# Optimization experiments

Hardware: AMD Instinct MI355X
Metric: run time of the kernel (lower is better)

Reference implementation:

```python
import jax, jax.numpy as jnp
import numpy as np

B, MT, D, H, DEPTH, FF = 1024, 64, 512, 8, 4, 2048
HD = D // H
N_OBJ, N_TRI = 8192, 10240
NUM_OBJ_VOCAB, NUM_PRED_VOCAB = 180, 47


def setup_inputs() -> dict:
    key = jax.random.key(0)
    ks = jax.random.split(key, 20)
    s = 0.02
    inp = {}
    inp["objs"] = jax.random.randint(ks[0], (N_OBJ,), 0, NUM_OBJ_VOCAB)
    inp["boxes"] = jax.random.uniform(ks[1], (N_OBJ, 4), dtype=jnp.float32)
    inp["triples"] = jax.random.randint(ks[2], (N_TRI, 3), 0, NUM_PRED_VOCAB)
    inp["obj_to_img"] = jnp.sort(jax.random.randint(ks[3], (N_OBJ,), 0, B))
    inp["triple_to_img"] = jnp.sort(jax.random.randint(ks[4], (N_TRI,), 0, B))
    inp["obj_emb"] = jax.random.normal(ks[5], (NUM_OBJ_VOCAB, D), jnp.float32) * s
    inp["pred_emb"] = jax.random.normal(ks[6], (NUM_PRED_VOCAB, D), jnp.float32) * s
    inp["bw1"] = jax.random.normal(ks[7], (4, D), jnp.float32) * s
    inp["bb1"] = jnp.zeros((D,), jnp.float32)
    inp["blg"] = jnp.ones((D,), jnp.float32)
    inp["blb"] = jnp.zeros((D,), jnp.float32)
    inp["bw2"] = jax.random.normal(ks[8], (D, D), jnp.float32) * s
    inp["bb2"] = jnp.zeros((D,), jnp.float32)
    inp["ln1g"] = jnp.ones((DEPTH, D), jnp.float32)
    inp["ln1b"] = jnp.zeros((DEPTH, D), jnp.float32)
    inp["wq"] = jax.random.normal(ks[9], (DEPTH, D, D), jnp.float32) * s
    inp["bq"] = jnp.zeros((DEPTH, D), jnp.float32)
    inp["wk"] = jax.random.normal(ks[10], (DEPTH, D, D), jnp.float32) * s
    inp["bk"] = jnp.zeros((DEPTH, D), jnp.float32)
    inp["wv"] = jax.random.normal(ks[11], (DEPTH, D, D), jnp.float32) * s
    inp["bv"] = jnp.zeros((DEPTH, D), jnp.float32)
    inp["wo"] = jax.random.normal(ks[12], (DEPTH, D, D), jnp.float32) * s
    inp["bo"] = jnp.zeros((DEPTH, D), jnp.float32)
    inp["ln2g"] = jnp.ones((DEPTH, D), jnp.float32)
    inp["ln2b"] = jnp.zeros((DEPTH, D), jnp.float32)
    inp["wf1"] = jax.random.normal(ks[13], (DEPTH, D, FF), jnp.float32) * s
    inp["bf1"] = jnp.zeros((DEPTH, FF), jnp.float32)
    inp["wf2"] = jax.random.normal(ks[14], (DEPTH, FF, D), jnp.float32) * s
    inp["bf2"] = jnp.zeros((DEPTH, D), jnp.float32)
    return inp


def _ln(x, g, b):
    m = x.mean(-1, keepdims=True)
    v = x.var(-1, keepdims=True)
    return (x - m) / jnp.sqrt(v + 1e-5) * g + b


def _forward(boxes, obj_emb, pred_emb, bw1, bb1, blg, blb, bw2, bb2,
             ln1g, ln1b, wq, bq, wk, bk, wv, bv, wo, bo, ln2g, ln2b,
             wf1, bf1, wf2, bf2, objs, triples, triple_to_img):
    # object tokens: embedding + box MLP (Linear -> LN -> GELU -> Linear)
    h = _ln(boxes @ bw1 + bb1, blg, blb)
    box_feat = jax.nn.gelu(h, approximate=False) @ bw2 + bb2
    obj_tok = obj_emb[objs] + box_feat  # (N_OBJ, D)

    s_idx, p_idx, o_idx = triples[:, 0], triples[:, 1], triples[:, 2]
    trip_tok = jnp.stack([obj_tok[s_idx], pred_emb[p_idx], obj_tok[o_idx]], axis=1)  # (T, 3, D)

    # vectorized ragged -> padded scatter (replaces per-image python loop)
    T = triples.shape[0]
    first = jnp.searchsorted(triple_to_img, jnp.arange(B))  # start of each image's segment
    pos = jnp.arange(T) - first[triple_to_img]               # rank of triple within its image
    slots = pos[:, None] * 3 + jnp.arange(3)[None, :]        # (T, 3) token slot per s/p/o
    imgs = jnp.broadcast_to(triple_to_img[:, None], slots.shape).reshape(-1)
    slot_c = jnp.where(slots < MT, slots, MT).reshape(-1)    # overflow -> dummy slot MT (truncation)
    tokens = jnp.zeros((B, MT + 1, D), boxes.dtype).at[imgs, slot_c].set(
        trip_tok.reshape(-1, D))[:, :MT]                     # (B, MT, D)
    mask = jnp.zeros((B, MT + 1), bool).at[imgs, slot_c].set(True)[:, :MT]  # (B, MT)

    x = tokens
    kmask = mask[:, None, None, :]  # (B,1,1,MT) valid-key mask
    scale = 1.0 / float(HD) ** 0.5
    for l in range(DEPTH):
        # pre-norm self-attention with key padding mask
        h = _ln(x, ln1g[l], ln1b[l])
        q = (h @ wq[l] + bq[l]).reshape(B, MT, H, HD)
        k = (h @ wk[l] + bk[l]).reshape(B, MT, H, HD)
        v = (h @ wv[l] + bv[l]).reshape(B, MT, H, HD)
        sc = jnp.einsum('bqhd,bkhd->bhqk', q, k) * scale
        sc = jnp.where(kmask, sc, -1e9)
        a = jax.nn.softmax(sc, axis=-1)
        attn = jnp.einsum('bhqk,bkhd->bqhd', a, v).reshape(B, MT, D)
        x = x + attn @ wo[l] + bo[l]
        # pre-norm FFN with exact GELU
        h = _ln(x, ln2g[l], ln2b[l])
        x = x + jax.nn.gelu(h @ wf1[l] + bf1[l], approximate=False) @ wf2[l] + bf2[l]
    return x


def reference(objs, boxes, triples, obj_to_img, triple_to_img, obj_emb, pred_emb,
              bw1, bb1, blg, blb, bw2, bb2, ln1g, ln1b, wq, bq, wk, bk, wv, bv,
              wo, bo, ln2g, ln2b, wf1, bf1, wf2, bf2):
    del obj_to_img  # only used in torch to derive batch_size; B is static here
    return _forward(boxes, obj_emb, pred_emb, bw1, bb1, blg, blb, bw2, bb2,
                    ln1g, ln1b, wq, bq, wk, bk, wv, bv, wo, bo, ln2g, ln2b,
                    wf1, bf1, wf2, bf2, objs, triples, triple_to_img)
```

## Files before the change

### kernel.cpp

```cpp
#include <hip/hip_runtime.h>

typedef unsigned short u16;
typedef __attribute__((ext_vector_type(8))) short s16x8;
typedef __attribute__((ext_vector_type(4))) float f32x4;

#define NB    1024
#define MTOK  64
#define DM    512
#define NHD   8
#define HDIM  64
#define FFD   2048
#define NOBJ  8192
#define NTRI  10240

__device__ __forceinline__ float bfu2f(u16 u) { return __uint_as_float(((unsigned)u) << 16); }
__device__ __forceinline__ u16 f2bfu(float f) {
  unsigned u = __float_as_uint(f);
  u += 0x7FFFu + ((u >> 16) & 1u);
  return (u16)(u >> 16);
}
__device__ __forceinline__ float gelu_exact(float x) {
  return 0.5f * x * (1.0f + erff(x * 0.70710678118654752440f));
}

__global__ void transpose_dd_kernel(const float* __restrict__ wq, const float* __restrict__ wk,
                                    const float* __restrict__ wv, const float* __restrict__ wo,
                                    u16* __restrict__ wqkvt, u16* __restrict__ wot) {
  __shared__ u16 tile[32][33];
  int l = blockIdx.z >> 2, w = blockIdx.z & 3;
  const float* src = (w == 0 ? wq : w == 1 ? wk : w == 2 ? wv : wo) + (size_t)l * 262144;
  u16* dst = (w < 3) ? (wqkvt + (size_t)l * 786432 + (size_t)w * 262144) : (wot + (size_t)l * 262144);
  int c0 = blockIdx.x * 32, r0 = blockIdx.y * 32;
  int tx = threadIdx.x, ty = threadIdx.y;
  #pragma unroll
  for (int i = 0; i < 4; i++)
    tile[ty + i * 8][tx] = f2bfu(src[(size_t)(r0 + ty + i * 8) * 512 + c0 + tx]);
  __syncthreads();
  #pragma unroll
  for (int i = 0; i < 4; i++)
    dst[(size_t)(c0 + ty + i * 8) * 512 + r0 + tx] = tile[tx][ty + i * 8];
}

__global__ void transpose_gen_kernel(const float* __restrict__ src, u16* __restrict__ dst,
                                     int R, int C) {
  __shared__ u16 tile[32][33];
  size_t mat = blockIdx.z;
  const float* s = src + mat * (size_t)R * C;
  u16* d = dst + mat * (size_t)R * C;
  int c0 = blockIdx.x * 32, r0 = blockIdx.y * 32;
  int tx = threadIdx.x, ty = threadIdx.y;
  #pragma unroll
  for (int i = 0; i < 4; i++)
    tile[ty + i * 8][tx] = f2bfu(s[(size_t)(r0 + ty + i * 8) * C + c0 + tx]);
  __syncthreads();
  #pragma unroll
  for (int i = 0; i < 4; i++)
    d[(size_t)(c0 + ty + i * 8) * R + r0 + tx] = tile[tx][ty + i * 8];
}

__global__ void concat_bias_kernel(const float* __restrict__ bq, const float* __restrict__ bk,
                                   const float* __restrict__ bv, float* __restrict__ bqkv) {
  int i = blockIdx.x * 256 + threadIdx.x;
  int l = i / 1536, j = i - l * 1536;
  int w = j >> 9, d = j & 511;
  const float* s = (w == 0) ? bq : (w == 1 ? bk : bv);
  bqkv[i] = s[l * 512 + d];
}

__global__ void first_kernel(const int* __restrict__ tti, int* __restrict__ first) {
  int b = threadIdx.x;
  int lo = 0, hi = NTRI;
  while (lo < hi) { int mid = (lo + hi) >> 1; if (tti[mid] < b) lo = mid + 1; else hi = mid; }
  first[b] = lo;
}

__global__ __launch_bounds__(256) void boxmlp_kernel(
    const int* __restrict__ objs, const float* __restrict__ boxes,
    const float* __restrict__ bw1, const float* __restrict__ bb1,
    const float* __restrict__ blg, const float* __restrict__ blb,
    const float* __restrict__ bw2, const float* __restrict__ bb2,
    const float* __restrict__ obj_emb, float* __restrict__ obj_tok) {
  __shared__ float hbuf[16][512];
  int tid = threadIdx.x;
  int base = blockIdx.x * 16;
  for (int o = 0; o < 16; o++) {
    int obj = base + o;
    float b0 = boxes[obj * 4 + 0], b1 = boxes[obj * 4 + 1];
    float b2 = boxes[obj * 4 + 2], b3 = boxes[obj * 4 + 3];
    for (int d = tid; d < 512; d += 256)
      hbuf[o][d] = bb1[d] + b0 * bw1[d] + b1 * bw1[512 + d] + b2 * bw1[1024 + d] + b3 * bw1[1536 + d];
  }
  __syncthreads();
  int wave = tid >> 6, lane = tid & 63;
  for (int oo = 0; oo < 4; oo++) {
    int o = wave * 4 + oo;
    float v[8], s = 0.f, ss = 0.f;
    #pragma unroll
    for (int e = 0; e < 8; e++) { v[e] = hbuf[o][lane * 8 + e]; s += v[e]; ss += v[e] * v[e]; }
    for (int off = 32; off > 0; off >>= 1) { s += __shfl_xor(s, off); ss += __shfl_xor(ss, off); }
    float mean = s * (1.0f / 512.0f);
    float var = ss * (1.0f / 512.0f) - mean * mean;
    float rstd = rsqrtf(var + 1e-5f);
    #pragma unroll
    for (int e = 0; e < 8; e++) {
      int d = lane * 8 + e;
      float g = (v[e] - mean) * rstd * blg[d] + blb[d];
      hbuf[o][d] = gelu_exact(g);
    }
  }
  __syncthreads();
  float acc0[16], acc1[16];
  #pragma unroll
  for (int o = 0; o < 16; o++) { acc0[o] = 0.f; acc1[o] = 0.f; }
  int d0 = tid, d1 = tid + 256;
  for (int k = 0; k < 512; k += 4) {
    float w0[4], w1[4];
    #pragma unroll
    for (int kk = 0; kk < 4; kk++) { w0[kk] = bw2[(k + kk) * 512 + d0]; w1[kk] = bw2[(k + kk) * 512 + d1]; }
    #pragma unroll
    for (int o = 0; o < 16; o++) {
      float4 hv = *(const float4*)&hbuf[o][k];
      acc0[o] += hv.x * w0[0] + hv.y * w0[1] + hv.z * w0[2] + hv.w * w0[3];
      acc1[o] += hv.x * w1[0] + hv.y * w1[1] + hv.z * w1[2] + hv.w * w1[3];
    }
  }
  #pragma unroll
  for (int o = 0; o < 16; o++) {
    int obj = base + o;
    int e = objs[obj];
    obj_tok[(size_t)obj * 512 + d0] = acc0[o] + bb2[d0] + obj_emb[(size_t)e * 512 + d0];
    obj_tok[(size_t)obj * 512 + d1] = acc1[o] + bb2[d1] + obj_emb[(size_t)e * 512 + d1];
  }
}

__global__ __launch_bounds__(128) void scatter_kernel(
    const int* __restrict__ triples, const int* __restrict__ tti,
    const int* __restrict__ first, const float* __restrict__ obj_tok,
    const float* __restrict__ pred_emb, float* __restrict__ x,
    unsigned char* __restrict__ maskb) {
  int t = blockIdx.x / 3, j = blockIdx.x - t * 3;
  int b = tti[t];
  int pos = t - first[b];
  int slot = pos * 3 + j;
  if (slot >= MTOK) return;
  int dst_row = b * MTOK + slot;
  int d = threadIdx.x * 4;
  float4 val;
  if (j == 1) {
    int p = triples[t * 3 + 1];
    val = *(const float4*)(pred_emb + (size_t)p * 512 + d);
  } else {
    int oi = triples[t * 3 + (j == 0 ? 0 : 2)];
    val = *(const float4*)(obj_tok + (size_t)oi * 512 + d);
  }
  *(float4*)(x + (size_t)dst_row * 512 + d) = val;
  if (threadIdx.x == 0) maskb[dst_row] = 1;
}

__global__ __launch_bounds__(256) void ln_kernel(
    const float* __restrict__ x, u16* __restrict__ out,
    const float* __restrict__ gg, const float* __restrict__ bb) {
  int row = blockIdx.x * 4 + (threadIdx.x >> 6);
  int lane = threadIdx.x & 63;
  const float* xr = x + (size_t)row * DM + lane * 8;
  float4 a = *(const float4*)xr;
  float4 c = *(const float4*)(xr + 4);
  float v[8] = {a.x, a.y, a.z, a.w, c.x, c.y, c.z, c.w};
  float s = 0.f, ss = 0.f;
  #pragma unroll
  for (int e = 0; e < 8; e++) { s += v[e]; ss += v[e] * v[e]; }
  for (int off = 32; off > 0; off >>= 1) { s += __shfl_xor(s, off); ss += __shfl_xor(ss, off); }
  float mean = s * (1.0f / 512.0f);
  float var = ss * (1.0f / 512.0f) - mean * mean;
  float rstd = rsqrtf(var + 1e-5f);
  int dbase = lane * 8;
  unsigned pk[4];
  #pragma unroll
  for (int p = 0; p < 4; p++) {
    float y0 = (v[2 * p] - mean) * rstd * gg[dbase + 2 * p] + bb[dbase + 2 * p];
    float y1 = (v[2 * p + 1] - mean) * rstd * gg[dbase + 2 * p + 1] + bb[dbase + 2 * p + 1];
    pk[p] = (unsigned)f2bfu(y0) | ((unsigned)f2bfu(y1) << 16);
  }
  uint4 o; o.x = pk[0]; o.y = pk[1]; o.z = pk[2]; o.w = pk[3];
  *(uint4*)(out + (size_t)row * DM + dbase) = o;
}

template <int MODE>
__global__ __launch_bounds__(256, 3) void gemm_kernel(
    const u16* __restrict__ A, const u16* __restrict__ Wt,
    const float* __restrict__ bias, float* __restrict__ resid,
    u16* __restrict__ outb, int M, int N, int K, int nb_n) {
  __shared__ u16 aT[128 * 64];
  __shared__ u16 bT[128 * 64];
  const int tid = threadIdx.x;
  const int wave = tid >> 6, lane = tid & 63;
  const int l15 = lane & 15, q4 = lane >> 4;
  const int wm = (wave >> 1) * 64, wn = (wave & 1) * 64;

  const int L = blockIdx.x;
  const int xg = L & 7, g = L >> 3;
  const int cblk = g % nb_n;
  const int pblk = xg + 8 * (g / nb_n);
  const int m0 = pblk * 128;
  const int n0 = cblk * 128;

  const int lrow = lane >> 3;
  const int scol = (((lane & 7) ^ lrow) << 3);
  const int swz = l15 & 7;

  f32x4 zero4 = {0.f, 0.f, 0.f, 0.f};
  f32x4 acc[4][4];
  #pragma unroll
  for (int i = 0; i < 4; i++)
    #pragma unroll
    for (int j = 0; j < 4; j++) acc[i][j] = zero4;

  for (int k0 = 0; k0 < K; k0 += 64) {
    __syncthreads();
    #pragma unroll
    for (int i = 0; i < 4; i++) {
      const int chunk = i * 4 + wave;
      const int row = chunk * 8 + lrow;
      __builtin_amdgcn_global_load_lds(
          (const __attribute__((address_space(1))) unsigned*)(A + (size_t)(m0 + row) * K + k0 + scol),
          (__attribute__((address_space(3))) unsigned*)(aT + chunk * 512), 16, 0, 0);
      __builtin_amdgcn_global_load_lds(
          (const __attribute__((address_space(1))) unsigned*)(Wt + (size_t)(n0 + row) * K + k0 + scol),
          (__attribute__((address_space(3))) unsigned*)(bT + chunk * 512), 16, 0, 0);
    }
    __syncthreads();
    #pragma unroll
    for (int kk = 0; kk < 64; kk += 32) {
      const int colA = (((kk >> 3) + q4) ^ swz) << 3;
      s16x8 fb[4], fa[4];
      #pragma unroll
      for (int j = 0; j < 4; j++)
        fb[j] = *(const s16x8*)(bT + (wn + j * 16 + l15) * 64 + colA);
      #pragma unroll
      for (int i = 0; i < 4; i++)
        fa[i] = *(const s16x8*)(aT + (wm + i * 16 + l15) * 64 + colA);
      #pragma unroll
      for (int i = 0; i < 4; i++)
        #pragma unroll
        for (int j = 0; j < 4; j++)
          acc[i][j] = __builtin_amdgcn_mfma_f32_16x16x32_bf16(fa[i], fb[j], acc[i][j], 0, 0, 0);
    }
  }

  #pragma unroll
  for (int i = 0; i < 4; i++) {
    #pragma unroll
    for (int j = 0; j < 4; j++) {
      int gn = n0 + wn + j * 16 + l15;
      float bv = bias[gn];
      #pragma unroll
      for (int r = 0; r < 4; r++) {
        int gm = m0 + wm + i * 16 + q4 * 4 + r;
        float v = acc[i][j][r] + bv;
        size_t off = (size_t)gm * N + gn;
        if (MODE == 0) outb[off] = f2bfu(v);
        else if (MODE == 1) resid[off] += v;
        else outb[off] = f2bfu(gelu_exact(v));
      }
    }
  }
}

__global__ __launch_bounds__(128) void attn_kernel(
    const u16* __restrict__ qkv, const unsigned char* __restrict__ maskb,
    u16* __restrict__ attnb) {
  __shared__ u16 vt_s[2][MTOK * 72];
  __shared__ u16 sP_s[2][MTOK * 72];
  __shared__ float maskf[MTOK];

  const int tid = threadIdx.x;
  const int wave = tid >> 6, lane = tid & 63;
  const int l15 = lane & 15, q4 = lane >> 4;
  const int b = blockIdx.x >> 2;
  const int h = ((blockIdx.x & 3) << 1) + wave;
  u16* vtw = vt_s[wave];
  u16* sw = sP_s[wave];

  if (tid < MTOK) maskf[tid] = maskb[b * MTOK + tid] ? 0.0f : -1e9f;

  {
    const u16* vrow = qkv + (size_t)(b * MTOK + lane) * 1536 + 1024 + h * HDIM;
    #pragma unroll
    for (int c8 = 0; c8 < 8; ++c8) {
      s16x8 v8 = *(const s16x8*)(vrow + c8 * 8);
      #pragma unroll
      for (int e = 0; e < 8; ++e)
        vtw[(c8 * 8 + e) * 72 + lane] = (u16)v8[e];
    }
  }
  __syncthreads();

  f32x4 zero4 = {0.f, 0.f, 0.f, 0.f};
  f32x4 acc[4][4];
  #pragma unroll
  for (int i = 0; i < 4; i++)
    #pragma unroll
    for (int j = 0; j < 4; j++) acc[i][j] = zero4;

  const u16* qbase = qkv + h * HDIM;
  const u16* kbase = qkv + 512 + h * HDIM;
  #pragma unroll
  for (int kk = 0; kk < HDIM; kk += 32) {
    s16x8 fa[4], fb[4];
    #pragma unroll
    for (int t = 0; t < 4; t++) {
      fa[t] = *(const s16x8*)(qbase + (size_t)(b * MTOK + t * 16 + l15) * 1536 + kk + q4 * 8);
      fb[t] = *(const s16x8*)(kbase + (size_t)(b * MTOK + t * 16 + l15) * 1536 + kk + q4 * 8);
    }
    #pragma unroll
    for (int i = 0; i < 4; i++)
      #pragma unroll
      for (int j = 0; j < 4; j++)
        acc[i][j] = __builtin_amdgcn_mfma_f32_16x16x32_bf16(fa[i], fb[j], acc[i][j], 0, 0, 0);
  }

  float mk[4];
  #pragma unroll
  for (int j = 0; j < 4; j++) mk[j] = maskf[j * 16 + l15];

  #pragma unroll
  for (int i = 0; i < 4; i++) {
    #pragma unroll
    for (int r = 0; r < 4; r++) {
      float mx = -3.0e38f;
      #pragma unroll
      for (int j = 0; j < 4; j++) {
        float s = acc[i][j][r] * 0.125f + mk[j];
        acc[i][j][r] = s;
        mx = fmaxf(mx, s);
      }
      mx = fmaxf(mx, __shfl_xor(mx, 1));
      mx = fmaxf(mx, __shfl_xor(mx, 2));
      mx = fmaxf(mx, __shfl_xor(mx, 4));
      mx = fmaxf(mx, __shfl_xor(mx, 8));
      float sum = 0.f;
      #pragma unroll
      for (int j = 0; j < 4; j++) {
        float e = __expf(acc[i][j][r] - mx);
        acc[i][j][r] = e;
        sum += e;
      }
      sum += __shfl_xor(sum, 1);
      sum += __shfl_xor(sum, 2);
      sum += __shfl_xor(sum, 4);
      sum += __shfl_xor(sum, 8);
      float inv = 1.0f / sum;
      int row = i * 16 + q4 * 4 + r;
      #pragma unroll
      for (int j = 0; j < 4; j++)
        sw[row * 72 + j * 16 + l15] = f2bfu(acc[i][j][r] * inv);
    }
  }
  __syncthreads();

  f32x4 oacc[4][4];
  #pragma unroll
  for (int i = 0; i < 4; i++)
    #pragma unroll
    for (int j = 0; j < 4; j++) oacc[i][j] = zero4;
  #pragma unroll
  for (int kk = 0; kk < MTOK; kk += 32) {
    s16x8 fa[4], fb[4];
    #pragma unroll
    for (int t = 0; t < 4; t++) {
      fa[t] = *(const s16x8*)(sw + (t * 16 + l15) * 72 + kk + q4 * 8);
      fb[t] = *(const s16x8*)(vtw + (t * 16 + l15) * 72 + kk + q4 * 8);
    }
    #pragma unroll
    for (int i = 0; i < 4; i++)
      #pragma unroll
      for (int j = 0; j < 4; j++)
        oacc[i][j] = __builtin_amdgcn_mfma_f32_16x16x32_bf16(fa[i], fb[j], oacc[i][j], 0, 0, 0);
  }
  #pragma unroll
  for (int i = 0; i < 4; i++)
    #pragma unroll
    for (int j = 0; j < 4; j++)
      #pragma unroll
      for (int r = 0; r < 4; r++)
        attnb[(size_t)(b * MTOK + i * 16 + q4 * 4 + r) * DM + h * HDIM + j * 16 + l15] =
            f2bfu(oacc[i][j][r]);
}

extern "C" void kernel_launch(void* const* d_in, const int* in_sizes, int n_in,
                              void* d_out, int out_size, void* d_ws, size_t ws_size,
                              hipStream_t stream) {
  (void)in_sizes; (void)n_in; (void)out_size; (void)ws_size;

  const int*   objs     = (const int*)  d_in[0];
  const float* boxes    = (const float*)d_in[1];
  const int*   triples  = (const int*)  d_in[2];
  const int*   tti      = (const int*)  d_in[4];
  const float* obj_emb  = (const float*)d_in[5];
  const float* pred_emb = (const float*)d_in[6];
  const float* bw1      = (const float*)d_in[7];
  const float* bb1      = (const float*)d_in[8];
  const float* blg      = (const float*)d_in[9];
  const float* blb      = (const float*)d_in[10];
  const float* bw2      = (const float*)d_in[11];
  const float* bb2      = (const float*)d_in[12];
  const float* ln1g     = (const float*)d_in[13];
  const float* ln1b     = (const float*)d_in[14];
  const float* wq       = (const float*)d_in[15];
  const float* bq       = (const float*)d_in[16];
  const float* wk       = (const float*)d_in[17];
  const float* bk       = (const float*)d_in[18];
  const float* wv       = (const float*)d_in[19];
  const float* bv       = (const float*)d_in[20];
  const float* wo       = (const float*)d_in[21];
  const float* bo       = (const float*)d_in[22];
  const float* ln2g     = (const float*)d_in[23];
  const float* ln2b     = (const float*)d_in[24];
  const float* wf1      = (const float*)d_in[25];
  const float* bf1      = (const float*)d_in[26];
  const float* wf2      = (const float*)d_in[27];
  const float* bf2      = (const float*)d_in[28];

  float* x = (float*)d_out;

  char* w = (char*)d_ws;
  u16* h_bf    = (u16*)w;   w += 67108864;
  u16* big     = (u16*)w;   w += 268435456;
  float* obj_tok = (float*)w; w += 16777216;
  u16* wqkvt   = (u16*)w;   w += 6291456;
  u16* wot     = (u16*)w;   w += 2097152;
  u16* wf1t    = (u16*)w;   w += 8388608;
  u16* wf2t    = (u16*)w;   w += 8388608;
  float* bqkv  = (float*)w; w += 24576;
  int* first   = (int*)w;   w += 4096;
  unsigned char* maskb = (unsigned char*)w; w += 65536;

  u16* qkv_bf  = big;
  u16* attn_bf = big + 100663296UL;
  u16* ff1_bf  = big;

  hipMemsetAsync(x, 0, 134217728UL, stream);
  hipMemsetAsync(maskb, 0, 65536, stream);

  transpose_dd_kernel<<<dim3(16, 16, 16), dim3(32, 8), 0, stream>>>(wq, wk, wv, wo, wqkvt, wot);
  transpose_gen_kernel<<<dim3(64, 16, 4), dim3(32, 8), 0, stream>>>(wf1, wf1t, 512, 2048);
  transpose_gen_kernel<<<dim3(16, 64, 4), dim3(32, 8), 0, stream>>>(wf2, wf2t, 2048, 512);
  concat_bias_kernel<<<24, 256, 0, stream>>>(bq, bk, bv, bqkv);
  first_kernel<<<1, 1024, 0, stream>>>(tti, first);
  boxmlp_kernel<<<512, 256, 0, stream>>>(objs, boxes, bw1, bb1, blg, blb, bw2, bb2, obj_emb, obj_tok);
  scatter_kernel<<<NTRI * 3, 128, 0, stream>>>(triples, tti, first, obj_tok, pred_emb, x, maskb);

  for (int l = 0; l < 4; l++) {
    ln_kernel<<<16384, 256, 0, stream>>>(x, h_bf, ln1g + l * 512, ln1b + l * 512);
    gemm_kernel<0><<<512 * 12, 256, 0, stream>>>(h_bf, wqkvt + (size_t)l * 786432,
                                                 bqkv + l * 1536, nullptr, qkv_bf,
                                                 65536, 1536, 512, 12);
    attn_kernel<<<4096, 128, 0, stream>>>(qkv_bf, maskb, attn_bf);
    gemm_kernel<1><<<512 * 4, 256, 0, stream>>>(attn_bf, wot + (size_t)l * 262144,
                                                bo + l * 512, x, nullptr,
                                                65536, 512, 512, 4);
    ln_kernel<<<16384, 256, 0, stream>>>(x, h_bf, ln2g + l * 512, ln2b + l * 512);
    gemm_kernel<2><<<512 * 16, 256, 0, stream>>>(h_bf, wf1t + (size_t)l * 1048576,
                                                 bf1 + l * 2048, nullptr, ff1_bf,
                                                 65536, 2048, 512, 16);
    gemm_kernel<1><<<512 * 4, 256, 0, stream>>>(ff1_bf, wf2t + (size_t)l * 1048576,
                                                bf2 + l * 512, x, nullptr,
                                                65536, 512, 2048, 4);
  }
}
```

Baseline: 3.531 ms.

## Stage GEMM epilogue through shared memory for coalesced vector stores

The GEMM epilogue now writes the accumulator tile into shared memory and then issues coalesced 16-byte global stores (bf16 outputs) or float4 read-modify-write on the residual, replacing scattered 2-byte/4-byte per-element stores. The shared buffer is enlarged slightly to hold a padded output tile. Launch bounds are raised to 4 blocks per SM, which tightens the register budget. The change adds extra barriers and LDS traffic, and the tighter register limit risks spills.

```diff
diff --git a/kernel.cpp b/kernel.cpp
--- a/kernel.cpp
+++ b/kernel.cpp
@@ -186,12 +186,13 @@
 }
 
 template <int MODE>
-__global__ __launch_bounds__(256, 3) void gemm_kernel(
+__global__ __launch_bounds__(256, 4) void gemm_kernel(
     const u16* __restrict__ A, const u16* __restrict__ Wt,
     const float* __restrict__ bias, float* __restrict__ resid,
     u16* __restrict__ outb, int M, int N, int K, int nb_n) {
-  __shared__ u16 aT[128 * 64];
-  __shared__ u16 bT[128 * 64];
+  __shared__ __align__(16) u16 smem[17408];
+  u16* aT = smem;
+  u16* bT = smem + 8192;
   const int tid = threadIdx.x;
   const int wave = tid >> 6, lane = tid & 63;
   const int l15 = lane & 15, q4 = lane >> 4;
@@ -247,21 +248,59 @@
     }
   }
 
-  #pragma unroll
-  for (int i = 0; i < 4; i++) {
-    #pragma unroll
-    for (int j = 0; j < 4; j++) {
-      int gn = n0 + wn + j * 16 + l15;
-      float bv = bias[gn];
-      #pragma unroll
-      for (int r = 0; r < 4; r++) {
-        int gm = m0 + wm + i * 16 + q4 * 4 + r;
-        float v = acc[i][j][r] + bv;
-        size_t off = (size_t)gm * N + gn;
-        if (MODE == 0) outb[off] = f2bfu(v);
-        else if (MODE == 1) resid[off] += v;
-        else outb[off] = f2bfu(gelu_exact(v));
+  __syncthreads();
+  if (MODE == 1) {
+    float* sf = (float*)smem;
+    #pragma unroll
+    for (int p = 0; p < 2; ++p) {
+      if ((wm >> 6) == p) {
+        #pragma unroll
+        for (int i = 0; i < 4; i++)
+          #pragma unroll
+          for (int j = 0; j < 4; j++) {
+            int lc = wn + j * 16 + l15;
+            float bv = bias[n0 + lc];
+            #pragma unroll
+            for (int r = 0; r < 4; r++)
+              sf[(i * 16 + q4 * 4 + r) * 132 + lc] = acc[i][j][r] + bv;
+          }
       }
+      __syncthreads();
+      #pragma unroll
+      for (int s = 0; s < 8; ++s) {
+        int idx = s * 256 + tid;
+        int row = idx >> 5;
+        int c4 = (idx & 31) * 4;
+        float* gp = resid + (size_t)(m0 + p * 64 + row) * N + n0 + c4;
+        float4 t = *(float4*)gp;
+        float4 l = *(const float4*)&sf[row * 132 + c4];
+        t.x += l.x; t.y += l.y; t.z += l.z; t.w += l.w;
+        *(float4*)gp = t;
+      }
+      __syncthreads();
+    }
+  } else {
+    #pragma unroll
+    for (int i = 0; i < 4; i++)
+      #pragma unroll
+      for (int j = 0; j < 4; j++) {
+        int lc = wn + j * 16 + l15;
+        float bv = bias[n0 + lc];
+        #pragma unroll
+        for (int r = 0; r < 4; r++) {
+          float v = acc[i][j][r] + bv;
+          if (MODE == 2) v = gelu_exact(v);
+          smem[(wm + i * 16 + q4 * 4 + r) * 136 + lc] = f2bfu(v);
+        }
+      }
+    __syncthreads();
+    const int c8 = (tid & 15) * 8;
+    const int r4 = tid >> 4;
+    #pragma unroll
+    for (int s = 0; s < 8; ++s) {
+      int row = s * 16 + r4;
+      s16x8 val = *(const s16x8*)&smem[row * 136 + c8];
+      *(s16x8*)(outb + (size_t)(m0 + row) * N + n0 + c8) = val;
     }
   }
 }
```

Result: faster. 3.326 ms (-5.8%).

## Vectorize GEMM epilogue via swapped MFMA operands, fast GELU, raise occupancy

Applied to the files above, without the earlier changes.

The MFMA operands are swapped so each lane holds four consecutive output columns of one row. This lets the epilogue issue float4 bias loads, float4 read-modify-write on the residual, and packed 8-byte bf16 stores instead of scattered scalar accesses. Exact erf-based GELU is replaced with the Abramowitz-Stegun polynomial using a hardware reciprocal and fast exp, which adds small approximation error. The launch-bounds occupancy hint is raised from 3 to 4 blocks, which may force register spills.

```diff
diff --git a/kernel.cpp b/kernel.cpp
--- a/kernel.cpp
+++ b/kernel.cpp
@@ -20,7 +20,16 @@
   return (u16)(u >> 16);
 }
 __device__ __forceinline__ float gelu_exact(float x) {
-  return 0.5f * x * (1.0f + erff(x * 0.70710678118654752440f));
+  float z = fabsf(x) * 0.70710678118654752440f;
+  float t = __builtin_amdgcn_rcpf(__builtin_fmaf(0.3275911f, z, 1.0f));
+  float p = t * (0.254829592f +
+            t * (-0.284496736f +
+            t * (1.421413741f +
+            t * (-1.453152027f +
+            t * 1.061405429f))));
+  float e = 1.0f - p * __expf(-z * z);
+  e = copysignf(e, x);
+  return 0.5f * x * (1.0f + e);
 }
 
 __global__ void transpose_dd_kernel(const float* __restrict__ wq, const float* __restrict__ wk,
@@ -186,12 +195,13 @@
 }
 
 template <int MODE>
-__global__ __launch_bounds__(256, 3) void gemm_kernel(
+__global__ __launch_bounds__(256, 4) void gemm_kernel(
     const u16* __restrict__ A, const u16* __restrict__ Wt,
     const float* __restrict__ bias, float* __restrict__ resid,
     u16* __restrict__ outb, int M, int N, int K, int nb_n) {
-  __shared__ u16 aT[128 * 64];
-  __shared__ u16 bT[128 * 64];
+  __shared__ __align__(16) u16 smem[16384];
+  u16* aT = smem;
+  u16* bT = smem + 8192;
   const int tid = threadIdx.x;
   const int wave = tid >> 6, lane = tid & 63;
   const int l15 = lane & 15, q4 = lane >> 4;
@@ -243,24 +253,35 @@
       for (int i = 0; i < 4; i++)
         #pragma unroll
         for (int j = 0; j < 4; j++)
-          acc[i][j] = __builtin_amdgcn_mfma_f32_16x16x32_bf16(fa[i], fb[j], acc[i][j], 0, 0, 0);
-    }
-  }
-
-  #pragma unroll
-  for (int i = 0; i < 4; i++) {
-    #pragma unroll
-    for (int j = 0; j < 4; j++) {
-      int gn = n0 + wn + j * 16 + l15;
-      float bv = bias[gn];
-      #pragma unroll
-      for (int r = 0; r < 4; r++) {
-        int gm = m0 + wm + i * 16 + q4 * 4 + r;
-        float v = acc[i][j][r] + bv;
-        size_t off = (size_t)gm * N + gn;
-        if (MODE == 0) outb[off] = f2bfu(v);
-        else if (MODE == 1) resid[off] += v;
-        else outb[off] = f2bfu(gelu_exact(v));
+          acc[i][j] = __builtin_amdgcn_mfma_f32_16x16x32_bf16(fb[j], fa[i], acc[i][j], 0, 0, 0);
+    }
+  }
+
+  #pragma unroll
+  for (int j = 0; j < 4; j++) {
+    const int gn0 = n0 + wn + j * 16 + q4 * 4;
+    const float4 bv = *(const float4*)&bias[gn0];
+    #pragma unroll
+    for (int i = 0; i < 4; i++) {
+      const int gm = m0 + wm + i * 16 + l15;
+      float v0 = acc[i][j][0] + bv.x;
+      float v1 = acc[i][j][1] + bv.y;
+      float v2 = acc[i][j][2] + bv.z;
+      float v3 = acc[i][j][3] + bv.w;
+      if (MODE == 1) {
+        float* gp = resid + (size_t)gm * N + gn0;
+        float4 t = *(float4*)gp;
+        t.x += v0; t.y += v1; t.z += v2; t.w += v3;
+        *(float4*)gp = t;
+      } else {
+        if (MODE == 2) {
+          v0 = gelu_exact(v0); v1 = gelu_exact(v1);
+          v2 = gelu_exact(v2); v3 = gelu_exact(v3);
+        }
+        uint2 pk;
+        pk.x = (unsigned)f2bfu(v0) | ((unsigned)f2bfu(v1) << 16);
+        pk.y = (unsigned)f2bfu(v2) | ((unsigned)f2bfu(v3) << 16);
+        *(uint2*)(outb + (size_t)gm * N + gn0) = pk;
       }
     }
   }
```

Result: faster. 3.448 ms (-2.4%).
